# Kernel optimization log

Hardware: AMD Instinct MI355X
Metric: run time of the kernel (lower is better)

## Reference

```python
import jax, jax.numpy as jnp
import numpy as np


def setup_inputs() -> dict:
    key = jax.random.key(0)
    k1, k2 = jax.random.split(key)
    B, D, H, W = 8, 64, 384, 512
    input1 = jax.random.normal(k1, (B, D, H, W), dtype=jnp.float32)
    input2 = jax.random.normal(k2, (B, 2, H, W), dtype=jnp.float32)  # flow (u, v) in pixels
    return {"input1": input1, "input2": input2}


def reference(input1, input2):
    # Equivalent of: grid = base_grid + 2*flow/(size-1); F.grid_sample(input1, grid,
    # mode='bilinear', padding_mode='border', align_corners=True).
    # With align_corners=True the normalized grid unmaps exactly to pixel coords
    # fx = x + u, fy = y + v; border padding clips coords to the image rectangle.
    B, D, H, W = input1.shape
    dt = input1.dtype
    u = input2[:, 0]  # (B, H, W) horizontal flow
    v = input2[:, 1]  # (B, H, W) vertical flow

    fx = jnp.arange(W, dtype=dt)[None, None, :] + u
    fy = jnp.arange(H, dtype=dt)[None, :, None] + v
    # padding_mode='border': clip sample coordinates to valid range
    fx = jnp.clip(fx, 0.0, W - 1)
    fy = jnp.clip(fy, 0.0, H - 1)

    x0 = jnp.floor(fx)
    y0 = jnp.floor(fy)
    wx = fx - x0  # bilinear weights, (B, H, W)
    wy = fy - y0
    x0i = x0.astype(jnp.int32)
    y0i = y0.astype(jnp.int32)
    x1i = jnp.minimum(x0i + 1, W - 1)
    y1i = jnp.minimum(y0i + 1, H - 1)

    img = jnp.transpose(input1, (0, 2, 3, 1))  # (B, H, W, D) channels-last for gather
    bidx = jnp.arange(B)[:, None, None]

    def gather(yi, xi):
        return img[bidx, yi, xi]  # (B, H, W, D)

    out = (gather(y0i, x0i) * ((1 - wy) * (1 - wx))[..., None]
           + gather(y0i, x1i) * ((1 - wy) * wx)[..., None]
           + gather(y1i, x0i) * (wy * (1 - wx))[..., None]
           + gather(y1i, x1i) * (wy * wx)[..., None])
    return jnp.transpose(out, (0, 3, 1, 2))  # back to (B, D, H, W)
```

## Files before the change

kernel.cpp:

```cpp
#include <hip/hip_runtime.h>

#define Bdim 8
#define Ddim 64
#define Hdim 384
#define Wdim 512

#define TH 16
#define TW 64
#define TILES_W (Wdim / TW)
#define TILES_H (Hdim / TH)
#define TILES_PER_B (TILES_W * TILES_H)

#define YH 32
#define XW 96
#define LSTRIDE 104


__global__ __launch_bounds__(256, 4) void resample2d_kernel(
    const float* __restrict__ img,
    const float* __restrict__ flow,
    float* __restrict__ out)
{
    __shared__ float S[YH * LSTRIDE];

    const int HW = Hdim * Wdim;
    int bid = blockIdx.x;
    int b   = bid / TILES_PER_B;
    int s   = bid - b * TILES_PER_B;
    int tr  = s >> 3;
    int tc  = s & 7;
    int ty  = tr * TH, tx = tc * TW;

    int lane = threadIdx.x & 63;
    int wv   = threadIdx.x >> 6;
    int w    = tx + lane;

    int YLO = max(0, min(ty - 8,  Hdim - YH));
    int XLO = max(0, min(tx - 16, Wdim - XW));

    const float* fb = flow + (size_t)b * 2 * HW;
    const float* ib = img  + (size_t)b * Ddim * HW;
    float*       ob = out  + (size_t)b * Ddim * HW;

    float w00[4], w01[4], w10[4], w11[4];
    int   lA[4], gA[4], oA[4];
    bool  ok[4];

    #pragma unroll
    for (int r = 0; r < 4; ++r) {
        int h  = ty + wv * 4 + r;
        int hw = h * Wdim + w;
        float u = __builtin_nontemporal_load(fb + hw);
        float v = __builtin_nontemporal_load(fb + HW + hw);

        float fx = fminf(fmaxf((float)w + u, 0.0f), (float)(Wdim - 1));
        float fy = fminf(fmaxf((float)h + v, 0.0f), (float)(Hdim - 1));
        int x0 = min((int)floorf(fx), Wdim - 2);
        int y0 = min((int)floorf(fy), Hdim - 2);
        float wx = fx - (float)x0;
        float wy = fy - (float)y0;

        w00[r] = (1.0f - wy) * (1.0f - wx);
        w01[r] = (1.0f - wy) * wx;
        w10[r] = wy * (1.0f - wx);
        w11[r] = wy * wx;

        gA[r] = y0 * Wdim + x0;
        lA[r] = (y0 - YLO) * LSTRIDE + (x0 - XLO);
        oA[r] = hw;
        ok[r] = (x0 >= XLO) & (x0 <= XLO + XW - 2) &
                (y0 >= YLO) & (y0 <= YLO + YH - 2);
    }

    int goff[3], loff[3];
    #pragma unroll
    for (int k = 0; k < 3; ++k) {
        int i   = (int)threadIdx.x + 256 * k;
        int row = i / 24;
        int c   = i - row * 24;
        goff[k] = (YLO + row) * Wdim + XLO + 4 * c;
        loff[k] = row * LSTRIDE + 4 * c;
    }

    auto LOADS = [&](int d, float4& s0, float4& s1, float4& s2) {
        const float* p = ib + (size_t)d * HW;
        s0 = *(const float4*)(p + goff[0]);
        s1 = *(const float4*)(p + goff[1]);
        s2 = *(const float4*)(p + goff[2]);
    };
    auto WRITE = [&](const float4& s0, const float4& s1, const float4& s2) {
        *(float4*)(&S[loff[0]]) = s0;
        *(float4*)(&S[loff[1]]) = s1;
        *(float4*)(&S[loff[2]]) = s2;
    };
    auto COMPUTE = [&](int d) {
        const float* p = ib + (size_t)d * HW;
        float*       o = ob + (size_t)d * HW;
        #pragma unroll
        for (int r = 0; r < 4; ++r) {
            float f00, f01, f10, f11;
            if (__builtin_expect((int)ok[r], 1)) {
                int a = lA[r];
                f00 = S[a];            f01 = S[a + 1];
                f10 = S[a + LSTRIDE];  f11 = S[a + LSTRIDE + 1];
            } else {
                const float* q = p + gA[r];
                float2 lo = *(const float2*)q;
                float2 hi = *(const float2*)(q + Wdim);
                f00 = lo.x; f01 = lo.y; f10 = hi.x; f11 = hi.y;
            }
            float res = f00 * w00[r] + f01 * w01[r]
                      + f10 * w10[r] + f11 * w11[r];
            __builtin_nontemporal_store(res, o + oA[r]);
        }
    };

    float4 a0, a1, a2, b0, b1, b2;
    LOADS(0, a0, a1, a2);
    for (int d = 0; d < Ddim; d += 2) {
        __syncthreads();
        WRITE(a0, a1, a2);
        LOADS(d + 1, b0, b1, b2);
        __syncthreads();
        COMPUTE(d);

        __syncthreads();
        WRITE(b0, b1, b2);
        if (d + 2 < Ddim) LOADS(d + 2, a0, a1, a2);
        __syncthreads();
        COMPUTE(d + 1);
    }
}

extern "C" void kernel_launch(void* const* d_in, const int* in_sizes, int n_in,
                              void* d_out, int out_size, void* d_ws, size_t ws_size,
                              hipStream_t stream) {
    const float* img  = (const float*)d_in[0];
    const float* flow = (const float*)d_in[1];
    float* out = (float*)d_out;

    const int total_blocks = Bdim * TILES_PER_B;
    dim3 block(256);
    dim3 grid(total_blocks);
    resample2d_kernel<<<grid, block, 0, stream>>>(img, flow, out);
}
```

Baseline: 773.5 us.

## Split channels across blocks and double-buffer LDS tile to halve barriers

Each block now handles a 16-channel slice instead of all 64, multiplying the grid by four, and the channel slice is chosen from the block index so neighbouring blocks share a spatial tile. Shared memory is double-buffered (two tiles), so each channel step needs one barrier instead of two, and the channel loop is fully unrolled. Launch bounds are raised to 6 blocks per SM. The trade-off is that flow loading and bilinear weight computation are repeated for each channel chunk, and the larger LDS footprint per block may limit occupancy.

```diff
diff --git a/kernel.cpp b/kernel.cpp
--- a/kernel.cpp
+++ b/kernel.cpp
@@ -9,27 +9,33 @@
 #define TW 64
 #define TILES_W (Wdim / TW)
 #define TILES_H (Hdim / TH)
-#define TILES_PER_B (TILES_W * TILES_H)
+#define DBLK 16
+#define DCHUNKS (Ddim / DBLK)
 
 #define YH 32
 #define XW 96
 #define LSTRIDE 104
+#define LDS_FLOATS (YH * LSTRIDE)
 
 
-__global__ __launch_bounds__(256, 4) void resample2d_kernel(
+__global__ __launch_bounds__(256, 6) void resample2d_kernel(
     const float* __restrict__ img,
     const float* __restrict__ flow,
     float* __restrict__ out)
 {
-    __shared__ float S[YH * LSTRIDE];
+    __shared__ float SA[LDS_FLOATS];
+    __shared__ float SB[LDS_FLOATS];
 
     const int HW = Hdim * Wdim;
     int bid = blockIdx.x;
-    int b   = bid / TILES_PER_B;
-    int s   = bid - b * TILES_PER_B;
-    int tr  = s >> 3;
-    int tc  = s & 7;
+    int tc  = bid & 7;
+    int t1  = bid >> 3;
+    int dc  = t1 & 3;
+    int t2  = t1 >> 2;
+    int tr  = t2 % TILES_H;
+    int b   = t2 / TILES_H;
     int ty  = tr * TH, tx = tc * TW;
+    int d0  = dc * DBLK;
 
     int lane = threadIdx.x & 63;
     int wv   = threadIdx.x >> 6;
@@ -88,12 +94,12 @@
         s1 = *(const float4*)(p + goff[1]);
         s2 = *(const float4*)(p + goff[2]);
     };
-    auto WRITE = [&](const float4& s0, const float4& s1, const float4& s2) {
-        *(float4*)(&S[loff[0]]) = s0;
-        *(float4*)(&S[loff[1]]) = s1;
-        *(float4*)(&S[loff[2]]) = s2;
+    auto WRITE = [&](float* S, const float4& s0, const float4& s1, const float4& s2) {
+        *(float4*)(S + loff[0]) = s0;
+        *(float4*)(S + loff[1]) = s1;
+        *(float4*)(S + loff[2]) = s2;
     };
-    auto COMPUTE = [&](int d) {
+    auto COMPUTE = [&](int d, const float* S) {
         const float* p = ib + (size_t)d * HW;
         float*       o = ob + (size_t)d * HW;
         #pragma unroll
@@ -116,19 +122,22 @@
     };
 
     float4 a0, a1, a2, b0, b1, b2;
-    LOADS(0, a0, a1, a2);
-    for (int d = 0; d < Ddim; d += 2) {
+    LOADS(d0, a0, a1, a2);
+    WRITE(SA, a0, a1, a2);
+    LOADS(d0 + 1, b0, b1, b2);
+    __syncthreads();
+
+    #pragma unroll
+    for (int dd = 0; dd < DBLK; dd += 2) {
+        WRITE(SB, b0, b1, b2);
+        if (dd + 2 < DBLK) LOADS(d0 + dd + 2, a0, a1, a2);
+        COMPUTE(d0 + dd, SA);
         __syncthreads();
-        WRITE(a0, a1, a2);
-        LOADS(d + 1, b0, b1, b2);
+
+        if (dd + 2 < DBLK) WRITE(SA, a0, a1, a2);
+        if (dd + 3 < DBLK) LOADS(d0 + dd + 3, b0, b1, b2);
+        COMPUTE(d0 + dd + 1, SB);
         __syncthreads();
-        COMPUTE(d);
-
-        __syncthreads();
-        WRITE(b0, b1, b2);
-        if (d + 2 < Ddim) LOADS(d + 2, a0, a1, a2);
-        __syncthreads();
-        COMPUTE(d + 1);
     }
 }
 
@@ -139,7 +148,7 @@
     const float* flow = (const float*)d_in[1];
     float* out = (float*)d_out;
 
-    const int total_blocks = Bdim * TILES_PER_B;
+    const int total_blocks = Bdim * TILES_H * DCHUNKS * TILES_W;
     dim3 block(256);
     dim3 grid(total_blocks);
     resample2d_kernel<<<grid, block, 0, stream>>>(img, flow, out);
```

After: 760.7 us. Within noise of the previous version (-1.7%).
